# Kernel optimization log

Hardware: AMD Instinct MI355X
Metric: run time of the kernel (lower is better)

Reference implementation:

```python
import jax, jax.numpy as jnp
import numpy as np

UP = 2
KSIZE = 3
RES = 64
LRELU_SLOPE = 0.2
ACT_GAIN = float(np.sqrt(2.0))  # def_gain of 'lrelu' in bias_act


def _setup_filter():
    # upfirdn2d.setup_filter([1,3,3,1]): normalize, make separable 2D filter
    f = jnp.array([1.0, 3.0, 3.0, 1.0], dtype=jnp.float32)
    f = f / jnp.sum(f)
    return jnp.outer(f, f)  # [4,4]


def _upfirdn2d_up2(x, f2):
    # Zero-insertion upsample by 2 + pad + FIR filter, gain = up**2.
    # Torch path: zero-insert to 2H, pad (3,2), conv 4-tap -> 2H+2.
    # lhs_dilation gives 2H-1; absorbing the trailing inserted zero into the
    # right pad ((3,3) instead of (3,2)) is exactly equivalent.
    B, C, H, W = x.shape
    k = (f2 * (UP * UP)).astype(x.dtype)[None, None]  # [1,1,4,4] (symmetric, flip-invariant)
    k = jnp.tile(k, (C, 1, 1, 1))                     # depthwise [C,1,4,4]
    return jax.lax.conv_general_dilated(
        x, k, window_strides=(1, 1), padding=((3, 3), (3, 3)),
        lhs_dilation=(UP, UP),
        dimension_numbers=('NCHW', 'OIHW', 'NCHW'),
        feature_group_count=C)


def setup_inputs() -> dict:
    key = jax.random.key(0)
    ks = jax.random.split(key, 6)
    B, Cin, Cout, Wd = 16, 512, 512, 512
    Hin = RES // UP
    return {
        "x": jax.random.normal(ks[0], (B, Cin, Hin, Hin), jnp.float32),
        "w": jax.random.normal(ks[1], (B, Wd), jnp.float32),
        "affine_weight": jax.random.normal(ks[2], (Cin, Wd), jnp.float32),
        "affine_bias": jnp.ones((Cin,), jnp.float32),  # bias_init=1
        "weight": jax.random.normal(ks[3], (Cout, Cin, KSIZE, KSIZE), jnp.float32),
        "bias": jnp.zeros((Cout,), jnp.float32),
        "noise_const": jax.random.normal(ks[4], (RES, RES), jnp.float32),
        "noise_strength": jax.random.uniform(ks[5], (), jnp.float32),
    }


def reference(x, w, affine_weight, affine_bias, weight, bias, noise_const, noise_strength):
    B, Cin, Hin, Win = x.shape
    Cout = weight.shape[0]
    # affine: FullyConnectedLayer, weight_gain = 1/sqrt(w_dim), bias_init=1
    styles = w @ affine_weight.T * (1.0 / np.sqrt(w.shape[1])) + affine_bias  # [B,Cin]
    # modulate + demodulate (fused_modconv=True): per-sample weights
    wmod = weight[None] * styles[:, None, :, None, None]                     # [B,Cout,Cin,kh,kw]
    dcoef = jax.lax.rsqrt(jnp.sum(jnp.square(wmod), axis=(2, 3, 4)) + 1e-8)  # [B,Cout]
    wmod = wmod * dcoef[:, :, None, None, None]
    # up=2 -> flip_weight=False -> true convolution: flip spatial taps
    wmod = wmod[..., ::-1, ::-1]
    # conv2d_resample: upfirdn2d upsample first (pad = k//2 + (fw+up-1)//2 = 3), then VALID conv
    xu = _upfirdn2d_up2(x, _setup_filter())                                  # [B,Cin,66,66]
    xr = xu.reshape(1, B * Cin, xu.shape[2], xu.shape[3])
    wr = wmod.reshape(B * Cout, Cin, KSIZE, KSIZE)
    y = jax.lax.conv_general_dilated(
        xr, wr, window_strides=(1, 1), padding='VALID',
        dimension_numbers=('NCHW', 'OIHW', 'NCHW'),
        feature_group_count=B)
    y = y.reshape(B, Cout, RES, RES)
    # noise_mode='const': noise = noise_const * noise_strength
    y = y + noise_const * noise_strength
    # fused bias + lrelu + def_gain (gain=1, conv_clamp=None)
    y = jax.nn.leaky_relu(y + bias[None, :, None, None], LRELU_SLOPE) * ACT_GAIN
    return y
```

## Files before the change

kernel.cpp:

```cpp
#include <hip/hip_runtime.h>
#include <hip/hip_bf16.h>
#include <math.h>

#define CIN   512
#define COUT  512
#define NB    16
#define WD    512
#define HIN   32
#define HUP   66
#define RES   64
#define LRELU 0.2f
#define ACT_GAIN 1.4142135623730951f

typedef __attribute__((ext_vector_type(8))) short short8;
typedef __attribute__((ext_vector_type(4))) float float4v;

__global__ void styles2_kernel(const float* __restrict__ w,
                               const float* __restrict__ aw,
                               const float* __restrict__ ab,
                               float* __restrict__ styles) {
    int b = blockIdx.x;
    int cig = blockIdx.y;
    int lane = threadIdx.x & 63, wv = threadIdx.x >> 6;
    __shared__ float wsh[WD];
    for (int e = threadIdx.x; e < WD; e += 256) wsh[e] = w[b * WD + e];
    __syncthreads();
    for (int r = 0; r < 16; ++r) {
        int ci = cig * 64 + wv * 16 + r;
        const float* arow = aw + (size_t)ci * WD;
        float acc = 0.f;
        for (int k = lane; k < WD; k += 64) acc += arow[k] * wsh[k];
        for (int off = 32; off; off >>= 1) acc += __shfl_down(acc, off, 64);
        if (lane == 0)
            styles[b * CIN + ci] = acc * 0.04419417382415922f + ab[ci];
    }
}

__global__ void prep_weights(const float* __restrict__ weight,
                             float* __restrict__ wsq,
                             __hip_bfloat16* __restrict__ wb) {
    int idx = blockIdx.x * 256 + threadIdx.x;
    int co = idx & (COUT - 1);
    int ci = idx >> 9;
    const float* wp = weight + ((size_t)co * CIN + ci) * 9;
    int cc = ci >> 5, chi = (ci >> 3) & 3, clo = ci & 7;
    float s = 0.f;
#pragma unroll
    for (int t = 0; t < 9; ++t) {
        float v = wp[t];
        s += v * v;
        int tf = 8 - t;
        wb[((((size_t)cc * 9 + tf) * 4 + chi) * COUT + co) * 8 + clo] = __float2bfloat16(v);
    }
    wsq[(size_t)co * CIN + ci] = s;
}

__global__ void dcoef2_kernel(const float* __restrict__ styles,
                              const float* __restrict__ wsq,
                              float* __restrict__ dcoef) {
    int b = blockIdx.x;
    int cog = blockIdx.y;
    int lane = threadIdx.x & 63, wv = threadIdx.x >> 6;
    __shared__ float s2[CIN];
    for (int e = threadIdx.x; e < CIN; e += 256) {
        float s = styles[b * CIN + e];
        s2[e] = s * s;
    }
    __syncthreads();
    for (int r = 0; r < 16; ++r) {
        int co = cog * 64 + wv * 16 + r;
        const float* qrow = wsq + (size_t)co * CIN;
        float acc = 0.f;
        for (int k = lane; k < CIN; k += 64) acc += qrow[k] * s2[k];
        for (int off = 32; off; off >>= 1) acc += __shfl_down(acc, off, 64);
        if (lane == 0) dcoef[b * COUT + co] = rsqrtf(acc + 1e-8f);
    }
}

__global__ void upmod2_kernel(const float* __restrict__ x,
                              const float* __restrict__ styles,
                              __hip_bfloat16* __restrict__ xs2) {
    __shared__ float xt[128 * 68];
    __shared__ float ssh[128];
    const int oh = blockIdx.x;
    const int ci0 = blockIdx.y * 128;
    const int b = blockIdx.z;
    int m0, m1; float a0, a1;
    if (oh & 1) { m0 = (oh - 3) >> 1; a0 = 0.125f; m1 = (oh - 1) >> 1; a1 = 0.375f; }
    else        { m0 = (oh >> 1) - 1; a0 = 0.375f; m1 = (oh >> 1);     a1 = 0.125f; }
    if (threadIdx.x < 128) ssh[threadIdx.x] = styles[b * CIN + ci0 + threadIdx.x] * 4.0f;
    for (int e = threadIdx.x; e < 2048; e += 256) {
        int ci = e >> 4, sel = (e >> 3) & 1, iw4 = e & 7;
        int m = sel ? m1 : m0;
        float4v v = (float4v)0.f;
        if (m >= 0 && m < HIN)
            v = *(const float4v*)(x + ((size_t)(b * CIN + ci0 + ci) * HIN + m) * HIN + iw4 * 4);
        *(float4v*)(&xt[ci * 68 + sel * 32 + iw4 * 4]) = v;
    }
    __syncthreads();
    for (int e = threadIdx.x; e < 1056; e += 256) {
        int cig = e / 66;
        int ow = e - cig * 66;
        int n0i, n1i; float b0, b1;
        if (ow & 1) { n0i = (ow - 3) >> 1; b0 = 0.125f; n1i = (ow - 1) >> 1; b1 = 0.375f; }
        else        { n0i = (ow >> 1) - 1; b0 = 0.375f; n1i = (ow >> 1);     b1 = 0.125f; }
        bool c0 = (n0i >= 0) & (n0i < HIN);
        bool c1 = (n1i >= 0) & (n1i < HIN);
        short8 sv;
#pragma unroll
        for (int u = 0; u < 8; ++u) {
            int ci = cig * 8 + u;
            const float* base = &xt[ci * 68];
            float r0 = (c0 ? base[n0i] : 0.f) * b0 + (c1 ? base[n1i] : 0.f) * b1;
            float r1 = (c0 ? base[32 + n0i] : 0.f) * b0 + (c1 ? base[32 + n1i] : 0.f) * b1;
            float val = (a0 * r0 + a1 * r1) * ssh[ci];
            __hip_bfloat16 h = __float2bfloat16(val);
            sv[u] = *reinterpret_cast<const short*>(&h);
        }
        *reinterpret_cast<short8*>(
            xs2 + (((size_t)b * HUP + oh) * HUP + ow) * CIN + ci0 + cig * 8) = sv;
    }
}

#define ABUF 43008
#define BBUF 36864
#define BUFSZ (ABUF + BBUF)
#define LDS_TOT (2 * BUFSZ)

__global__ __launch_bounds__(512, 1) void conv_mfma(
        const __hip_bfloat16* __restrict__ xs2,
        const __hip_bfloat16* __restrict__ wb,
        const float* __restrict__ dcoef,
        const float* __restrict__ bias,
        const float* __restrict__ noise,
        const float* __restrict__ nstr,
        float* __restrict__ out)
{
    extern __shared__ __align__(16) char smem[];
    const int tid = threadIdx.x;
    const int lane = tid & 63;
    const int wid = tid >> 6;
    const int li = lane & 15;
    const int q = lane >> 4;
    const int mb = blockIdx.x;
    const int n0 = blockIdx.y * 64;
    const int b  = blockIdx.z;
    const int y0 = mb * 8;

    int a_goff[6];
#pragma unroll
    for (int k = 0; k < 6; ++k) {
        int n = wid + k * 8;
        int s = n * 64 + lane;
        if (s > 2639) s = 2639;
        int r = s / 264;
        int rem = s - r * 264;
        int chi = rem / 66;
        int col = rem - chi * 66;
        a_goff[k] = ((b * HUP + y0 + r) * HUP + col) * CIN + chi * 8;
    }
    int b_goff[5];
#pragma unroll
    for (int k = 0; k < 5; ++k) {
        int sl = wid + k * 8;
        b_goff[k] = (sl * COUT + n0 + lane) * 8;
    }

    float4v acc[4][4];
#pragma unroll
    for (int i = 0; i < 4; ++i)
#pragma unroll
        for (int j = 0; j < 4; ++j) acc[i][j] = (float4v)0.f;

    const char* xg = (const char*)xs2;
    const char* wg = (const char*)wb;

#define STAGE(CC, BUFB) do {                                                  \
        _Pragma("unroll")                                                     \
        for (int k = 0; k < 5; ++k) {                                         \
            int sl = wid + k * 8;                                             \
            if (sl < 36) {                                                    \
                long ge = (long)(b_goff[k] + (CC) * 147456);                  \
                __builtin_amdgcn_global_load_lds(                             \
                    (const __attribute__((address_space(1))) char*)(wg + ge * 2), \
                    (__attribute__((address_space(3))) char*)(smem + (BUFB) + ABUF + sl * 1024), \
                    16, 0, 0);                                                \
            }                                                                 \
        }                                                                     \
        _Pragma("unroll")                                                     \
        for (int k = 0; k < 6; ++k) {                                         \
            int n = wid + k * 8;                                              \
            if (n < 42) {                                                     \
                long ge = (long)(a_goff[k] + (CC) * 32);                      \
                __builtin_amdgcn_global_load_lds(                             \
                    (const __attribute__((address_space(1))) char*)(xg + ge * 2), \
                    (__attribute__((address_space(3))) char*)(smem + (BUFB) + n * 1024), \
                    16, 0, 0);                                                \
            }                                                                 \
        }                                                                     \
    } while (0)

#define COMPUTE(BUFB) do {                                                    \
        __builtin_amdgcn_s_setprio(1);                                        \
        _Pragma("unroll")                                                     \
        for (int t = 0; t < 9; ++t) {                                         \
            const int kh = t / 3, kw = t - kh * 3;                            \
            short8 bf[4];                                                     \
            _Pragma("unroll")                                                 \
            for (int j = 0; j < 4; ++j)                                       \
                bf[j] = *(const short8*)(smem + (BUFB) + ABUF +               \
                        (((t * 4 + q) * 64) + j * 16 + li) * 16);             \
            _Pragma("unroll")                                                 \
            for (int i = 0; i < 4; ++i) {                                     \
                short8 af = *(const short8*)(smem + (BUFB) +                  \
                        ((((wid + kh) * 4 + q) * 66) + (i * 16 + li + kw)) * 16); \
                _Pragma("unroll")                                             \
                for (int j = 0; j < 4; ++j)                                   \
                    acc[i][j] = __builtin_amdgcn_mfma_f32_16x16x32_bf16(      \
                        af, bf[j], acc[i][j], 0, 0, 0);                       \
            }                                                                 \
        }                                                                     \
        __builtin_amdgcn_s_setprio(0);                                        \
    } while (0)

#define SYNC() do {                                                           \
        asm volatile("s_waitcnt vmcnt(0)" ::: "memory");                      \
        __builtin_amdgcn_s_barrier();                                         \
    } while (0)

    STAGE(0, 0);
    SYNC();

#pragma unroll 1
    for (int cc = 0; cc < 16; cc += 2) {
        STAGE(cc + 1, BUFSZ);
        COMPUTE(0);
        SYNC();
        if (cc + 2 < 16) STAGE(cc + 2, 0);
        COMPUTE(BUFSZ);
        SYNC();
    }

#undef STAGE
#undef COMPUTE
#undef SYNC

    const float ns = nstr[0];
    const int row = y0 + wid;
#pragma unroll
    for (int j = 0; j < 4; ++j) {
        int cout = n0 + j * 16 + li;
        float dc = dcoef[b * COUT + cout];
        float bs = bias[cout];
        float* op = out + ((size_t)(b * COUT + cout) * RES + row) * RES;
#pragma unroll
        for (int i = 0; i < 4; ++i) {
            int colb = i * 16 + q * 4;
            float4v nz = *(const float4v*)(noise + row * RES + colb);
            float4v a = acc[i][j];
            float4v r;
            r.x = a.x * dc + nz.x * ns + bs;
            r.y = a.y * dc + nz.y * ns + bs;
            r.z = a.z * dc + nz.z * ns + bs;
            r.w = a.w * dc + nz.w * ns + bs;
            r.x = (r.x > 0.f ? r.x : LRELU * r.x) * ACT_GAIN;
            r.y = (r.y > 0.f ? r.y : LRELU * r.y) * ACT_GAIN;
            r.z = (r.z > 0.f ? r.z : LRELU * r.z) * ACT_GAIN;
            r.w = (r.w > 0.f ? r.w : LRELU * r.w) * ACT_GAIN;
            *(float4v*)(op + colb) = r;
        }
    }
}

extern "C" void kernel_launch(void* const* d_in, const int* in_sizes, int n_in,
                              void* d_out, int out_size, void* d_ws, size_t ws_size,
                              hipStream_t stream) {
    (void)in_sizes; (void)n_in; (void)out_size; (void)ws_size;
    const float* x     = (const float*)d_in[0];
    const float* w     = (const float*)d_in[1];
    const float* aw    = (const float*)d_in[2];
    const float* ab    = (const float*)d_in[3];
    const float* wt    = (const float*)d_in[4];
    const float* bias  = (const float*)d_in[5];
    const float* noise = (const float*)d_in[6];
    const float* nstr  = (const float*)d_in[7];
    float* out = (float*)d_out;

    static bool init = false;
    if (!init) {
        hipFuncSetAttribute(reinterpret_cast<const void*>(conv_mfma),
                            hipFuncAttributeMaxDynamicSharedMemorySize, LDS_TOT);
        init = true;
    }

    char* ws = (char*)d_ws;
    float* styles = (float*)ws;
    float* dcoef  = (float*)(ws + 32768);
    float* wsq    = (float*)(ws + 65536);
    __hip_bfloat16* wb  = (__hip_bfloat16*)(ws + 65536 + 1048576);
    __hip_bfloat16* xs2 = (__hip_bfloat16*)(ws + 65536 + 1048576 + 4718592);

    styles2_kernel<<<dim3(NB, 8), dim3(256), 0, stream>>>(w, aw, ab, styles);
    prep_weights<<<dim3(1024), dim3(256), 0, stream>>>(wt, wsq, wb);
    dcoef2_kernel<<<dim3(NB, 8), dim3(256), 0, stream>>>(styles, wsq, dcoef);
    upmod2_kernel<<<dim3(HUP, 4, NB), dim3(256), 0, stream>>>(x, styles, xs2);
    conv_mfma<<<dim3(8, 8, NB), dim3(512), LDS_TOT, stream>>>(
        xs2, wb, dcoef, bias, noise, nstr, out);
}
```

Measured before the change: 492.6 us.

## Switch conv to 32x32x16 MFMA tiles and stage upmod output through LDS

The conv kernel's inner product moves from 16x16x32 bf16 MFMA with a 4x4 fragment grid to 32x32x16 bf16 MFMA with a 2x2 grid. This reduces the number of LDS fragment reads per MFMA and the instruction count for the same tile. The epilogue is remapped to the 32x32 accumulator layout. Separately, the upsample/modulate kernel now writes its bf16 results to an LDS buffer and then stores them to global memory in channel-contiguous order, so writes coalesce better. The cost is extra LDS use and a barrier in that kernel.

```diff
diff --git a/kernel.cpp b/kernel.cpp
--- a/kernel.cpp
+++ b/kernel.cpp
@@ -14,6 +14,7 @@
 
 typedef __attribute__((ext_vector_type(8))) short short8;
 typedef __attribute__((ext_vector_type(4))) float float4v;
+typedef __attribute__((ext_vector_type(16))) float float16v;
 
 __global__ void styles2_kernel(const float* __restrict__ w,
                                const float* __restrict__ aw,
@@ -82,6 +83,7 @@
                               __hip_bfloat16* __restrict__ xs2) {
     __shared__ float xt[128 * 68];
     __shared__ float ssh[128];
+    __shared__ __align__(16) char ob[66 * 272];
     const int oh = blockIdx.x;
     const int ci0 = blockIdx.y * 128;
     const int b = blockIdx.z;
@@ -117,8 +119,14 @@
             __hip_bfloat16 h = __float2bfloat16(val);
             sv[u] = *reinterpret_cast<const short*>(&h);
         }
+        *reinterpret_cast<short8*>(ob + ow * 272 + cig * 16) = sv;
+    }
+    __syncthreads();
+    for (int e = threadIdx.x; e < 1056; e += 256) {
+        int ow = e >> 4, t16 = e & 15;
+        short8 v = *reinterpret_cast<const short8*>(ob + ow * 272 + t16 * 16);
         *reinterpret_cast<short8*>(
-            xs2 + (((size_t)b * HUP + oh) * HUP + ow) * CIN + ci0 + cig * 8) = sv;
+            xs2 + (((size_t)b * HUP + oh) * HUP + ow) * CIN + ci0 + t16 * 8) = v;
     }
 }
 
@@ -140,8 +148,8 @@
     const int tid = threadIdx.x;
     const int lane = tid & 63;
     const int wid = tid >> 6;
-    const int li = lane & 15;
-    const int q = lane >> 4;
+    const int li32 = lane & 31;
+    const int hi = lane >> 5;
     const int mb = blockIdx.x;
     const int n0 = blockIdx.y * 64;
     const int b  = blockIdx.z;
@@ -166,11 +174,11 @@
         b_goff[k] = (sl * COUT + n0 + lane) * 8;
     }
 
-    float4v acc[4][4];
-#pragma unroll
-    for (int i = 0; i < 4; ++i)
-#pragma unroll
-        for (int j = 0; j < 4; ++j) acc[i][j] = (float4v)0.f;
+    float16v acc[2][2];
+#pragma unroll
+    for (int i = 0; i < 2; ++i)
+#pragma unroll
+        for (int j = 0; j < 2; ++j) acc[i][j] = (float16v)0.f;
 
     const char* xg = (const char*)xs2;
     const char* wg = (const char*)wb;
@@ -205,19 +213,23 @@
         _Pragma("unroll")                                                     \
         for (int t = 0; t < 9; ++t) {                                         \
             const int kh = t / 3, kw = t - kh * 3;                            \
-            short8 bf[4];                                                     \
             _Pragma("unroll")                                                 \
-            for (int j = 0; j < 4; ++j)                                       \
-                bf[j] = *(const short8*)(smem + (BUFB) + ABUF +               \
-                        (((t * 4 + q) * 64) + j * 16 + li) * 16);             \
-            _Pragma("unroll")                                                 \
-            for (int i = 0; i < 4; ++i) {                                     \
-                short8 af = *(const short8*)(smem + (BUFB) +                  \
-                        ((((wid + kh) * 4 + q) * 66) + (i * 16 + li + kw)) * 16); \
+            for (int ks = 0; ks < 2; ++ks) {                                  \
+                short8 bfr[2];                                                \
                 _Pragma("unroll")                                             \
-                for (int j = 0; j < 4; ++j)                                   \
-                    acc[i][j] = __builtin_amdgcn_mfma_f32_16x16x32_bf16(      \
-                        af, bf[j], acc[i][j], 0, 0, 0);                       \
+                for (int nf = 0; nf < 2; ++nf)                                \
+                    bfr[nf] = *(const short8*)(smem + (BUFB) + ABUF +         \
+                            (((t * 4 + ks * 2 + hi) * 64) + nf * 32 + li32) * 16); \
+                _Pragma("unroll")                                             \
+                for (int mf = 0; mf < 2; ++mf) {                              \
+                    short8 af = *(const short8*)(smem + (BUFB) +              \
+                            ((((wid + kh) * 4 + ks * 2 + hi) * 66) +          \
+                             (mf * 32 + li32 + kw)) * 16);                    \
+                    _Pragma("unroll")                                         \
+                    for (int nf = 0; nf < 2; ++nf)                            \
+                        acc[mf][nf] = __builtin_amdgcn_mfma_f32_32x32x16_bf16(\
+                            af, bfr[nf], acc[mf][nf], 0, 0, 0);               \
+                }                                                             \
             }                                                                 \
         }                                                                     \
         __builtin_amdgcn_s_setprio(0);                                        \
@@ -248,26 +260,28 @@
     const float ns = nstr[0];
     const int row = y0 + wid;
 #pragma unroll
-    for (int j = 0; j < 4; ++j) {
-        int cout = n0 + j * 16 + li;
+    for (int nf = 0; nf < 2; ++nf) {
+        int cout = n0 + nf * 32 + li32;
         float dc = dcoef[b * COUT + cout];
         float bs = bias[cout];
         float* op = out + ((size_t)(b * COUT + cout) * RES + row) * RES;
 #pragma unroll
-        for (int i = 0; i < 4; ++i) {
-            int colb = i * 16 + q * 4;
-            float4v nz = *(const float4v*)(noise + row * RES + colb);
-            float4v a = acc[i][j];
-            float4v r;
-            r.x = a.x * dc + nz.x * ns + bs;
-            r.y = a.y * dc + nz.y * ns + bs;
-            r.z = a.z * dc + nz.z * ns + bs;
-            r.w = a.w * dc + nz.w * ns + bs;
-            r.x = (r.x > 0.f ? r.x : LRELU * r.x) * ACT_GAIN;
-            r.y = (r.y > 0.f ? r.y : LRELU * r.y) * ACT_GAIN;
-            r.z = (r.z > 0.f ? r.z : LRELU * r.z) * ACT_GAIN;
-            r.w = (r.w > 0.f ? r.w : LRELU * r.w) * ACT_GAIN;
-            *(float4v*)(op + colb) = r;
+        for (int mf = 0; mf < 2; ++mf) {
+#pragma unroll
+            for (int r2 = 0; r2 < 4; ++r2) {
+                int x0 = mf * 32 + hi * 4 + r2 * 8;
+                float4v nz = *(const float4v*)(noise + row * RES + x0);
+                float4v r;
+                r.x = acc[mf][nf][r2 * 4 + 0] * dc + nz.x * ns + bs;
+                r.y = acc[mf][nf][r2 * 4 + 1] * dc + nz.y * ns + bs;
+                r.z = acc[mf][nf][r2 * 4 + 2] * dc + nz.z * ns + bs;
+                r.w = acc[mf][nf][r2 * 4 + 3] * dc + nz.w * ns + bs;
+                r.x = (r.x > 0.f ? r.x : LRELU * r.x) * ACT_GAIN;
+                r.y = (r.y > 0.f ? r.y : LRELU * r.y) * ACT_GAIN;
+                r.z = (r.z > 0.f ? r.z : LRELU * r.z) * ACT_GAIN;
+                r.w = (r.w > 0.f ? r.w : LRELU * r.w) * ACT_GAIN;
+                *(float4v*)(op + x0) = r;
+            }
         }
     }
 }
```

Measured after the change: 519.0 us. 1.05x slower.
